# Performance work log

Hardware: AMD Instinct MI355X
Metric: run time of the kernel (lower is better)

## Reference

```python
import jax, jax.numpy as jnp
import numpy as np

N, H, D = 1024, 64, 3

def _lin(x, W, b=None):
    y = x @ W.T
    return y if b is None else y + b

def setup_inputs() -> dict:
    key = jax.random.key(0)
    ks = jax.random.split(key, 16)
    def gl(k, o, i):  # glorot-ish linear weight
        lim = (6.0 / (i + o)) ** 0.5
        return jax.random.uniform(k, (o, i), minval=-lim, maxval=lim, dtype=jnp.float32)
    inp = {
        "h": jax.random.normal(ks[0], (N, H), dtype=jnp.float32),
        "x": jax.random.uniform(ks[1], (N, D), dtype=jnp.float32),  # coords in [0, L)
        "L": jnp.float32(1.0),
        # edge MLP: (2H+2) -> H -> H, silu both layers
        "ew1": gl(ks[2], H, 2 * H + 2), "eb1": jnp.zeros((H,), jnp.float32),
        "ew2": gl(ks[3], H, H),         "eb2": jnp.zeros((H,), jnp.float32),
        # node MLP: 2H -> H -> H
        "nw1": gl(ks[4], H, 2 * H),     "nb1": jnp.zeros((H,), jnp.float32),
        "nw2": gl(ks[5], H, H),         "nb2": jnp.zeros((H,), jnp.float32),
        # coord path
        "chw": gl(ks[6], H, H),         "chb": jnp.zeros((H,), jnp.float32),
        "cww": 0.001 * gl(ks[7], 1, H),  # small-init, no bias
        # attention gate
        "aw": gl(ks[8], 1, H),          "ab": jnp.zeros((1,), jnp.float32),
    }
    return inp

COORDS_RANGE = 10.0

def reference(h, x, L, ew1, eb1, ew2, eb2, nw1, nb1, nw2, nb2, chw, chb, cww, aw, ab):
    act = jax.nn.silu
    n, hd = h.shape
    # --- coord2radial: toroidal log map, x_i - x_j wrapped to [-L/2, L/2) ---
    diff = jnp.remainder(x[:, None, :] - x[None, :, :] + 0.5 * L, L) - 0.5 * L  # (N,N,D)
    radial = jnp.sum(diff ** 2, axis=-1, keepdims=True)                          # (N,N,1)
    coord_diff = diff / (jnp.sqrt(radial + 1e-8) + 1.0)                          # (N,N,D)
    # --- edge model: MLP([h_i, h_j, r, r]) decomposed to avoid concat ---
    Wa, Wb = ew1[:, :hd], ew1[:, hd:2 * hd]
    wr = ew1[:, 2 * hd] + ew1[:, 2 * hd + 1]                                     # (H,)
    pre = (h @ Wa.T)[:, None, :] + (h @ Wb.T)[None, :, :] + radial * wr + eb1    # (N,N,H)
    edge = act(act(pre) @ ew2.T + eb2)                                           # (N,N,H)
    att = jax.nn.sigmoid(edge @ aw.T + ab)                                       # (N,N,1)
    edge = edge * att
    # --- coord model ---
    ch = act(edge @ chw.T + chb)                                                 # (N,N,H)
    w = jnp.tanh(ch @ cww.T) * COORDS_RANGE                                      # (N,N,1)
    delta = jnp.sum(coord_diff * w, axis=1)                                      # (N,D)
    x_new = jnp.remainder(x + delta, L)
    # --- node model ---
    agg = jnp.sum(edge, axis=1)                                                  # (N,H)
    pre_n = h @ nw1[:, :hd].T + agg @ nw1[:, hd:].T + nb1
    h_new = h + (act(pre_n) @ nw2.T + nb2)                                       # recurrent
    return (h_new, x_new)
```

## Files before the change

### kernel.cpp

```cpp
#include <hip/hip_runtime.h>

#define Nn 1024

typedef __attribute__((ext_vector_type(8))) short short8v;
typedef __attribute__((ext_vector_type(4))) float floatx4;

__device__ __forceinline__ float frcp(float v)  { return __builtin_amdgcn_rcpf(v); }
__device__ __forceinline__ float fsilu(float v) { return v * frcp(1.0f + __expf(-v)); }
__device__ __forceinline__ float fsig(float v)  { return frcp(1.0f + __expf(-v)); }
__device__ __forceinline__ float ftanh10(float v){ return 10.0f - 20.0f * frcp(__expf(2.0f * v) + 1.0f); }

__device__ __forceinline__ unsigned cvtpk(float lo, float hi) {
    unsigned r;
    asm("v_cvt_pk_bf16_f32 %0, %1, %2" : "=v"(r) : "v"(lo), "v"(hi));
    return r;
}

union I4S8 { int4 i; short8v s; };

__global__ __launch_bounds__(256) void precompute_kernel(
    const float* __restrict__ h, const float* __restrict__ ew1,
    const float* __restrict__ eb1, const float* __restrict__ nw1,
    const float* __restrict__ nb1, float* __restrict__ ha,
    float* __restrict__ hb, float* __restrict__ hn1)
{
    int t = blockIdx.x * 256 + threadIdx.x;
    int which = t >> 16;
    int rem = t & 65535;
    int i = rem >> 6, o = rem & 63;
    const float* hrow = h + i * 64;
    const float* wrow;
    float acc;
    if (which == 0)      { wrow = ew1 + o * 130;      acc = eb1[o]; }
    else if (which == 1) { wrow = ew1 + o * 130 + 64; acc = 0.0f;   }
    else                 { wrow = nw1 + o * 128;      acc = nb1[o]; }
    #pragma unroll
    for (int k = 0; k < 64; ++k) acc = fmaf(hrow[k], wrow[k], acc);
    if (which == 0)      ha[rem]  = acc;
    else if (which == 1) hb[rem]  = acc;
    else                 hn1[rem] = acc;
}

__global__ __launch_bounds__(256) __attribute__((amdgpu_waves_per_eu(3, 4)))
void edge_mfma_kernel(
    const float* __restrict__ x, const float* __restrict__ Lp,
    const float* __restrict__ ha, const float* __restrict__ hb,
    const float* __restrict__ ew1, const float* __restrict__ ew2,
    const float* __restrict__ eb2, const float* __restrict__ chw,
    const float* __restrict__ chb, const float* __restrict__ aw,
    const float* __restrict__ ab, const float* __restrict__ cww,
    float* __restrict__ agg, float* __restrict__ delta)
{
    __shared__ __align__(16) int4 Wlds[1024];
    __shared__ __align__(16) float cvec[384];
    __shared__ __align__(16) float xs[Nn * 3];
    __shared__ float redagg[4][64];
    __shared__ float sdel[4][3];

    const int tid  = threadIdx.x;
    const int wave = tid >> 6, lane = tid & 63;
    const int lr = lane & 15, g = lane >> 4;
    const int i0 = blockIdx.x;
    const int jbase = wave * 256;
    const int ghi  = g >> 1;
    const int selA = (lr + ((g & 1) << 5)) << 2;
    const int selB = selA + 64;
    const int4* WldsF = &Wlds[0];

    {
        const float4* xsrc = (const float4*)x;
        float4* xdst = (float4*)xs;
        xdst[tid] = xsrc[tid];
        xdst[tid + 256] = xsrc[tid + 256];
        xdst[tid + 512] = xsrc[tid + 512];
    }

    if (wave == 0) {
      #pragma unroll
      for (int kt = 0; kt < 2; ++kt)
        #pragma unroll
        for (int nt = 0; nt < 4; ++nt) {
          int n = nt * 16 + lr;
          int k0 = kt * 32 + g * 8;
          float4 lo = *(const float4*)(ew2 + n * 64 + k0);
          float4 hi = *(const float4*)(ew2 + n * 64 + k0 + 4);
          Wlds[(kt * 4 + nt) * 64 + lane] = make_int4(
              (int)cvtpk(lo.x, lo.y), (int)cvtpk(lo.z, lo.w),
              (int)cvtpk(hi.x, hi.y), (int)cvtpk(hi.z, hi.w));
          lo = *(const float4*)(chw + n * 64 + k0);
          hi = *(const float4*)(chw + n * 64 + k0 + 4);
          Wlds[512 + (kt * 4 + nt) * 64 + lane] = make_int4(
              (int)cvtpk(lo.x, lo.y), (int)cvtpk(lo.z, lo.w),
              (int)cvtpk(hi.x, hi.y), (int)cvtpk(hi.z, hi.w));
        }
    }
    if (tid < 64) {
      cvec[tid]       = eb2[tid];
      cvec[64 + tid]  = aw[tid];
      cvec[128 + tid] = chb[tid];
      cvec[192 + tid] = cww[tid];
      cvec[256 + tid] = ha[i0 * 64 + tid];
      cvec[320 + tid] = ew1[tid * 130 + 128] + ew1[tid * 130 + 129];
    }

    const float L = Lp[0], invL = frcp(L);
    const float ab0 = ab[0];

    floatx4 agg4[4];
    #pragma unroll
    for (int nt = 0; nt < 4; ++nt) agg4[nt] = (floatx4){0.f, 0.f, 0.f, 0.f};
    float dp0 = 0.f, dp1 = 0.f, dp2 = 0.f;

    __syncthreads();

    const float xi0 = xs[i0 * 3 + 0], xi1 = xs[i0 * 3 + 1], xi2 = xs[i0 * 3 + 2];

    float4 hpre0, hpre1, hpre2, hpre3;
    {
      const float* hn = hb + (jbase + lr) * 64 + g * 8;
      hpre0 = *(const float4*)(hn);
      hpre1 = *(const float4*)(hn + 4);
      hpre2 = *(const float4*)(hn + 32);
      hpre3 = *(const float4*)(hn + 36);
    }

    for (int jc = 0; jc < 16; ++jc) {
      unsigned lidx = (unsigned)lane;
      asm volatile("" : "+v"(lidx));
      unsigned cb = (unsigned)(g << 4);
      asm volatile("" : "+v"(cb));
      unsigned hbo = (unsigned)(g << 5);
      asm volatile("" : "+v"(hbo));
      const float* cvp = (const float*)((const char*)cvec + cb);
      const float* hvp = (const float*)((const char*)cvec + 1024 + hbo);

      float4 h0 = hpre0, h1 = hpre1, h2 = hpre2, h3 = hpre3;
      if (jc < 15) {
        const float* hn = hb + (jbase + (jc + 1) * 16 + lr) * 64 + g * 8;
        hpre0 = *(const float4*)(hn);
        hpre1 = *(const float4*)(hn + 4);
        hpre2 = *(const float4*)(hn + 32);
        hpre3 = *(const float4*)(hn + 36);
      }

      const int j = jbase + jc * 16 + lr;
      float xd0 = xi0 - xs[j * 3 + 0];
      float xd1 = xi1 - xs[j * 3 + 1];
      float xd2 = xi2 - xs[j * 3 + 2];
      float d0 = xd0 - L * floorf(fmaf(xd0, invL, 0.5f));
      float d1 = xd1 - L * floorf(fmaf(xd1, invL, 0.5f));
      float d2 = xd2 - L * floorf(fmaf(xd2, invL, 0.5f));
      float radial = d0 * d0 + d1 * d1 + d2 * d2;
      float cinv = frcp(__builtin_amdgcn_sqrtf(radial + 1e-8f) + 1.0f);
      float dx0 = d0 * cinv, dx1 = d1 * cinv, dx2 = d2 * cinv;

      short8v tf[2];
      {
        union { short8v s; unsigned u[4]; } pk;
        #pragma unroll
        for (int kt = 0; kt < 2; ++kt) {
          floatx4 ha0 = *(const floatx4*)(hvp + kt * 32);
          floatx4 ha1 = *(const floatx4*)(hvp + kt * 32 + 4);
          floatx4 wr0 = *(const floatx4*)(hvp + 64 + kt * 32);
          floatx4 wr1 = *(const floatx4*)(hvp + 64 + kt * 32 + 4);
          const float4& hA = kt ? h2 : h0;
          const float4& hB = kt ? h3 : h1;
          floatx4 p0, p1;
          p0[0] = fsilu(fmaf(radial, wr0[0], ha0[0]) + hA.x);
          p0[1] = fsilu(fmaf(radial, wr0[1], ha0[1]) + hA.y);
          p0[2] = fsilu(fmaf(radial, wr0[2], ha0[2]) + hA.z);
          p0[3] = fsilu(fmaf(radial, wr0[3], ha0[3]) + hA.w);
          p1[0] = fsilu(fmaf(radial, wr1[0], ha1[0]) + hB.x);
          p1[1] = fsilu(fmaf(radial, wr1[1], ha1[1]) + hB.y);
          p1[2] = fsilu(fmaf(radial, wr1[2], ha1[2]) + hB.z);
          p1[3] = fsilu(fmaf(radial, wr1[3], ha1[3]) + hB.w);
          pk.u[0] = cvtpk(p0[0], p0[1]); pk.u[1] = cvtpk(p0[2], p0[3]);
          pk.u[2] = cvtpk(p1[0], p1[1]); pk.u[3] = cvtpk(p1[2], p1[3]);
          tf[kt] = pk.s;
        }
      }

      floatx4 acc[4];
      #pragma unroll
      for (int nt = 0; nt < 4; ++nt) acc[nt] = *(const floatx4*)(cvp + nt * 16);
      #pragma unroll
      for (int kt = 0; kt < 2; ++kt)
        #pragma unroll
        for (int nt = 0; nt < 4; ++nt) {
          I4S8 wv; wv.i = WldsF[(kt * 4 + nt) * 64 + lidx];
          acc[nt] = __builtin_amdgcn_mfma_f32_16x16x32_bf16(wv.s, tf[kt], acc[nt], 0, 0, 0);
        }

      float p = 0.f;
      #pragma unroll
      for (int nt = 0; nt < 4; ++nt) {
        floatx4 awv = *(const floatx4*)(cvp + 64 + nt * 16);
        #pragma unroll
        for (int r = 0; r < 4; ++r) {
          float s = fsilu(acc[nt][r]);
          acc[nt][r] = s;
          p = fmaf(s, awv[r], p);
        }
      }
      p += __shfl_xor(p, 16); p += __shfl_xor(p, 32);
      const float att = fsig(p + ab0);

      unsigned Pq[4][2];
      #pragma unroll
      for (int nt = 0; nt < 4; ++nt) {
        float e0 = acc[nt][0] * att, e1 = acc[nt][1] * att;
        float e2 = acc[nt][2] * att, e3 = acc[nt][3] * att;
        agg4[nt][0] += e0; agg4[nt][1] += e1;
        agg4[nt][2] += e2; agg4[nt][3] += e3;
        Pq[nt][0] = cvtpk(e0, e1);
        Pq[nt][1] = cvtpk(e2, e3);
      }

      union { short8v s; int u[4]; } ef[2];
      #pragma unroll
      for (int kt2 = 0; kt2 < 2; ++kt2)
        #pragma unroll
        for (int w = 0; w < 4; ++w) {
          int sel = (w < 2) ? selA : selB;
          int v0 = __builtin_amdgcn_ds_bpermute(sel, (int)Pq[kt2 * 2][w & 1]);
          int v1 = __builtin_amdgcn_ds_bpermute(sel, (int)Pq[kt2 * 2 + 1][w & 1]);
          ef[kt2].u[w] = ghi ? v1 : v0;
        }

      #pragma unroll
      for (int nt = 0; nt < 4; ++nt) acc[nt] = *(const floatx4*)(cvp + 128 + nt * 16);
      #pragma unroll
      for (int kt2 = 0; kt2 < 2; ++kt2)
        #pragma unroll
        for (int nt = 0; nt < 4; ++nt) {
          I4S8 wv; wv.i = WldsF[512 + (kt2 * 4 + nt) * 64 + lidx];
          acc[nt] = __builtin_amdgcn_mfma_f32_16x16x32_bf16(wv.s, ef[kt2].s, acc[nt], 0, 0, 0);
        }

      float q = 0.f;
      #pragma unroll
      for (int nt = 0; nt < 4; ++nt) {
        floatx4 cwv = *(const floatx4*)(cvp + 192 + nt * 16);
        #pragma unroll
        for (int r = 0; r < 4; ++r)
          q = fmaf(fsilu(acc[nt][r]), cwv[r], q);
      }
      q += __shfl_xor(q, 16); q += __shfl_xor(q, 32);
      const float wvv = ftanh10(q);
      if (g == 0) {
        dp0 = fmaf(dx0, wvv, dp0);
        dp1 = fmaf(dx1, wvv, dp1);
        dp2 = fmaf(dx2, wvv, dp2);
      }
    }

    #pragma unroll
    for (int nt = 0; nt < 4; ++nt)
      #pragma unroll
      for (int r = 0; r < 4; ++r) {
        float v = agg4[nt][r];
        v += __shfl_xor(v, 1); v += __shfl_xor(v, 2);
        v += __shfl_xor(v, 4); v += __shfl_xor(v, 8);
        agg4[nt][r] = v;
      }
    if (lr == 0) {
      #pragma unroll
      for (int nt = 0; nt < 4; ++nt)
        *(floatx4*)&redagg[wave][nt * 16 + (g << 2)] = agg4[nt];
    }
    dp0 += __shfl_xor(dp0, 1); dp0 += __shfl_xor(dp0, 2); dp0 += __shfl_xor(dp0, 4); dp0 += __shfl_xor(dp0, 8);
    dp1 += __shfl_xor(dp1, 1); dp1 += __shfl_xor(dp1, 2); dp1 += __shfl_xor(dp1, 4); dp1 += __shfl_xor(dp1, 8);
    dp2 += __shfl_xor(dp2, 1); dp2 += __shfl_xor(dp2, 2); dp2 += __shfl_xor(dp2, 4); dp2 += __shfl_xor(dp2, 8);
    if (lane == 0) { sdel[wave][0] = dp0; sdel[wave][1] = dp1; sdel[wave][2] = dp2; }
    __syncthreads();
    if (tid < 64)
      agg[i0 * 64 + tid] = redagg[0][tid] + redagg[1][tid] + redagg[2][tid] + redagg[3][tid];
    else if (tid < 67) {
      int d = tid - 64;
      delta[i0 * 3 + d] = sdel[0][d] + sdel[1][d] + sdel[2][d] + sdel[3][d];
    }
}

__global__ __launch_bounds__(256) void node_fused_kernel(
    const float* __restrict__ h, const float* __restrict__ hn1,
    const float* __restrict__ agg, const float* __restrict__ nw1,
    const float* __restrict__ nw2, const float* __restrict__ nb2,
    const float* __restrict__ x, const float* __restrict__ delta,
    const float* __restrict__ Lp, float* __restrict__ outh,
    float* __restrict__ outx)
{
    __shared__ float sps[256];
    const int b = blockIdx.x, tid = threadIdx.x;
    const int gt = b * 256 + tid;
    const int i = gt >> 6, o = gt & 63;
    const float* arow = agg + i * 64;
    const float* wrow = nw1 + o * 128 + 64;
    float acc = hn1[gt];
    #pragma unroll
    for (int k = 0; k < 64; ++k) acc = fmaf(arow[k], wrow[k], acc);
    sps[tid] = fsilu(acc);
    __syncthreads();
    const float* srow = sps + (tid & ~63);
    const float* w2row = nw2 + o * 64;
    float acc2 = h[gt] + nb2[o];
    #pragma unroll
    for (int k = 0; k < 64; ++k) acc2 = fmaf(srow[k], w2row[k], acc2);
    outh[gt] = acc2;
    if (tid < 12) {
        int ii = b * 4 + tid / 3, d = tid % 3;
        float L = Lp[0];
        float v = x[ii * 3 + d] + delta[ii * 3 + d];
        outx[ii * 3 + d] = v - L * floorf(v * frcp(L));
    }
}

extern "C" void kernel_launch(void* const* d_in, const int* in_sizes, int n_in,
                              void* d_out, int out_size, void* d_ws, size_t ws_size,
                              hipStream_t stream) {
    const float* h   = (const float*)d_in[0];
    const float* x   = (const float*)d_in[1];
    const float* Lp  = (const float*)d_in[2];
    const float* ew1 = (const float*)d_in[3];
    const float* eb1 = (const float*)d_in[4];
    const float* ew2 = (const float*)d_in[5];
    const float* eb2 = (const float*)d_in[6];
    const float* nw1 = (const float*)d_in[7];
    const float* nb1 = (const float*)d_in[8];
    const float* nw2 = (const float*)d_in[9];
    const float* nb2 = (const float*)d_in[10];
    const float* chw = (const float*)d_in[11];
    const float* chb = (const float*)d_in[12];
    const float* cww = (const float*)d_in[13];
    const float* aw  = (const float*)d_in[14];
    const float* ab  = (const float*)d_in[15];

    float* ws    = (float*)d_ws;
    float* ha    = ws;
    float* hb    = ws + 65536;
    float* hn1   = ws + 131072;
    float* agg   = ws + 196608;
    float* delta = ws + 262144;

    float* outh = (float*)d_out;
    float* outx = outh + 65536;

    precompute_kernel<<<768, 256, 0, stream>>>(h, ew1, eb1, nw1, nb1, ha, hb, hn1);
    edge_mfma_kernel<<<1024, 256, 0, stream>>>(x, Lp, ha, hb, ew1, ew2, eb2, chw, chb,
                                               aw, ab, cww, agg, delta);
    node_fused_kernel<<<256, 256, 0, stream>>>(h, hn1, agg, nw1, nw2, nb2, x, delta,
                                               Lp, outh, outx);
}
```

Measured before the change: 93.31 us.

## Split edge kernel j-range across two blocks per row and drop LDS x staging

```diff
diff --git a/kernel.cpp b/kernel.cpp
--- a/kernel.cpp
+++ b/kernel.cpp
@@ -20,9 +20,8 @@
 
 __global__ __launch_bounds__(256) void precompute_kernel(
     const float* __restrict__ h, const float* __restrict__ ew1,
-    const float* __restrict__ eb1, const float* __restrict__ nw1,
-    const float* __restrict__ nb1, float* __restrict__ ha,
-    float* __restrict__ hb, float* __restrict__ hn1)
+    const float* __restrict__ eb1, float* __restrict__ ha,
+    float* __restrict__ hb)
 {
     int t = blockIdx.x * 256 + threadIdx.x;
     int which = t >> 16;
@@ -31,17 +30,15 @@
     const float* hrow = h + i * 64;
     const float* wrow;
     float acc;
-    if (which == 0)      { wrow = ew1 + o * 130;      acc = eb1[o]; }
-    else if (which == 1) { wrow = ew1 + o * 130 + 64; acc = 0.0f;   }
-    else                 { wrow = nw1 + o * 128;      acc = nb1[o]; }
+    if (which == 0) { wrow = ew1 + o * 130;      acc = eb1[o]; }
+    else            { wrow = ew1 + o * 130 + 64; acc = 0.0f;   }
     #pragma unroll
     for (int k = 0; k < 64; ++k) acc = fmaf(hrow[k], wrow[k], acc);
-    if (which == 0)      ha[rem]  = acc;
-    else if (which == 1) hb[rem]  = acc;
-    else                 hn1[rem] = acc;
-}
-
-__global__ __launch_bounds__(256) __attribute__((amdgpu_waves_per_eu(3, 4)))
+    if (which == 0) ha[rem] = acc;
+    else            hb[rem] = acc;
+}
+
+__global__ __launch_bounds__(256) __attribute__((amdgpu_waves_per_eu(4, 8)))
 void edge_mfma_kernel(
     const float* __restrict__ x, const float* __restrict__ Lp,
     const float* __restrict__ ha, const float* __restrict__ hb,
@@ -49,31 +46,23 @@
     const float* __restrict__ eb2, const float* __restrict__ chw,
     const float* __restrict__ chb, const float* __restrict__ aw,
     const float* __restrict__ ab, const float* __restrict__ cww,
-    float* __restrict__ agg, float* __restrict__ delta)
+    float* __restrict__ agg_parts, float* __restrict__ delta_parts)
 {
     __shared__ __align__(16) int4 Wlds[1024];
     __shared__ __align__(16) float cvec[384];
-    __shared__ __align__(16) float xs[Nn * 3];
     __shared__ float redagg[4][64];
     __shared__ float sdel[4][3];
 
     const int tid  = threadIdx.x;
     const int wave = tid >> 6, lane = tid & 63;
     const int lr = lane & 15, g = lane >> 4;
-    const int i0 = blockIdx.x;
-    const int jbase = wave * 256;
+    const int i0 = blockIdx.x >> 1;
+    const int half = blockIdx.x & 1;
+    const int jbase = half * 512 + wave * 128;
     const int ghi  = g >> 1;
     const int selA = (lr + ((g & 1) << 5)) << 2;
     const int selB = selA + 64;
     const int4* WldsF = &Wlds[0];
-
-    {
-        const float4* xsrc = (const float4*)x;
-        float4* xdst = (float4*)xs;
-        xdst[tid] = xsrc[tid];
-        xdst[tid + 256] = xsrc[tid + 256];
-        xdst[tid + 512] = xsrc[tid + 512];
-    }
 
     if (wave == 0) {
       #pragma unroll
@@ -113,7 +102,7 @@
 
     __syncthreads();
 
-    const float xi0 = xs[i0 * 3 + 0], xi1 = xs[i0 * 3 + 1], xi2 = xs[i0 * 3 + 2];
+    const float xi0 = x[i0 * 3 + 0], xi1 = x[i0 * 3 + 1], xi2 = x[i0 * 3 + 2];
 
     float4 hpre0, hpre1, hpre2, hpre3;
     {
@@ -124,7 +113,7 @@
       hpre3 = *(const float4*)(hn + 36);
     }
 
-    for (int jc = 0; jc < 16; ++jc) {
+    for (int jc = 0; jc < 8; ++jc) {
       unsigned lidx = (unsigned)lane;
       asm volatile("" : "+v"(lidx));
       unsigned cb = (unsigned)(g << 4);
@@ -135,7 +124,7 @@
       const float* hvp = (const float*)((const char*)cvec + 1024 + hbo);
 
       float4 h0 = hpre0, h1 = hpre1, h2 = hpre2, h3 = hpre3;
-      if (jc < 15) {
+      if (jc < 7) {
         const float* hn = hb + (jbase + (jc + 1) * 16 + lr) * 64 + g * 8;
         hpre0 = *(const float4*)(hn);
         hpre1 = *(const float4*)(hn + 4);
@@ -144,9 +133,9 @@
       }
 
       const int j = jbase + jc * 16 + lr;
-      float xd0 = xi0 - xs[j * 3 + 0];
-      float xd1 = xi1 - xs[j * 3 + 1];
-      float xd2 = xi2 - xs[j * 3 + 2];
+      float xd0 = xi0 - x[j * 3 + 0];
+      float xd1 = xi1 - x[j * 3 + 1];
+      float xd2 = xi2 - x[j * 3 + 2];
       float d0 = xd0 - L * floorf(fmaf(xd0, invL, 0.5f));
       float d1 = xd1 - L * floorf(fmaf(xd1, invL, 0.5f));
       float d2 = xd2 - L * floorf(fmaf(xd2, invL, 0.5f));
@@ -274,18 +263,21 @@
     if (lane == 0) { sdel[wave][0] = dp0; sdel[wave][1] = dp1; sdel[wave][2] = dp2; }
     __syncthreads();
     if (tid < 64)
-      agg[i0 * 64 + tid] = redagg[0][tid] + redagg[1][tid] + redagg[2][tid] + redagg[3][tid];
+      agg_parts[half * 65536 + i0 * 64 + tid] =
+          redagg[0][tid] + redagg[1][tid] + redagg[2][tid] + redagg[3][tid];
     else if (tid < 67) {
       int d = tid - 64;
-      delta[i0 * 3 + d] = sdel[0][d] + sdel[1][d] + sdel[2][d] + sdel[3][d];
+      delta_parts[half * 3072 + i0 * 3 + d] =
+          sdel[0][d] + sdel[1][d] + sdel[2][d] + sdel[3][d];
     }
 }
 
 __global__ __launch_bounds__(256) void node_fused_kernel(
-    const float* __restrict__ h, const float* __restrict__ hn1,
-    const float* __restrict__ agg, const float* __restrict__ nw1,
-    const float* __restrict__ nw2, const float* __restrict__ nb2,
-    const float* __restrict__ x, const float* __restrict__ delta,
+    const float* __restrict__ h, const float* __restrict__ agg0,
+    const float* __restrict__ agg1, const float* __restrict__ nw1,
+    const float* __restrict__ nb1, const float* __restrict__ nw2,
+    const float* __restrict__ nb2, const float* __restrict__ x,
+    const float* __restrict__ delta0, const float* __restrict__ delta1,
     const float* __restrict__ Lp, float* __restrict__ outh,
     float* __restrict__ outx)
 {
@@ -293,11 +285,16 @@
     const int b = blockIdx.x, tid = threadIdx.x;
     const int gt = b * 256 + tid;
     const int i = gt >> 6, o = gt & 63;
-    const float* arow = agg + i * 64;
-    const float* wrow = nw1 + o * 128 + 64;
-    float acc = hn1[gt];
-    #pragma unroll
-    for (int k = 0; k < 64; ++k) acc = fmaf(arow[k], wrow[k], acc);
+    const float* hrow = h + i * 64;
+    const float* w1a = nw1 + o * 128;
+    const float* a0 = agg0 + i * 64;
+    const float* a1 = agg1 + i * 64;
+    const float* w1b = nw1 + o * 128 + 64;
+    float acc = nb1[o];
+    #pragma unroll
+    for (int k = 0; k < 64; ++k) acc = fmaf(hrow[k], w1a[k], acc);
+    #pragma unroll
+    for (int k = 0; k < 64; ++k) acc = fmaf(a0[k] + a1[k], w1b[k], acc);
     sps[tid] = fsilu(acc);
     __syncthreads();
     const float* srow = sps + (tid & ~63);
@@ -309,7 +306,7 @@
     if (tid < 12) {
         int ii = b * 4 + tid / 3, d = tid % 3;
         float L = Lp[0];
-        float v = x[ii * 3 + d] + delta[ii * 3 + d];
+        float v = x[ii * 3 + d] + delta0[ii * 3 + d] + delta1[ii * 3 + d];
         outx[ii * 3 + d] = v - L * floorf(v * frcp(L));
     }
 }
@@ -334,19 +331,20 @@
     const float* aw  = (const float*)d_in[14];
     const float* ab  = (const float*)d_in[15];
 
-    float* ws    = (float*)d_ws;
-    float* ha    = ws;
-    float* hb    = ws + 65536;
-    float* hn1   = ws + 131072;
-    float* agg   = ws + 196608;
-    float* delta = ws + 262144;
+    float* ws     = (float*)d_ws;
+    float* ha     = ws;
+    float* hb     = ws + 65536;
+    float* agg0   = ws + 131072;
+    float* agg1   = ws + 196608;
+    float* delta0 = ws + 262144;
+    float* delta1 = ws + 265216;
 
     float* outh = (float*)d_out;
     float* outx = outh + 65536;
 
-    precompute_kernel<<<768, 256, 0, stream>>>(h, ew1, eb1, nw1, nb1, ha, hb, hn1);
-    edge_mfma_kernel<<<1024, 256, 0, stream>>>(x, Lp, ha, hb, ew1, ew2, eb2, chw, chb,
-                                               aw, ab, cww, agg, delta);
-    node_fused_kernel<<<256, 256, 0, stream>>>(h, hn1, agg, nw1, nw2, nb2, x, delta,
-                                               Lp, outh, outx);
-}
+    precompute_kernel<<<512, 256, 0, stream>>>(h, ew1, eb1, ha, hb);
+    edge_mfma_kernel<<<2048, 256, 0, stream>>>(x, Lp, ha, hb, ew1, ew2, eb2, chw, chb,
+                                               aw, ab, cww, ws + 131072, ws + 262144);
+    node_fused_kernel<<<256, 256, 0, stream>>>(h, agg0, agg1, nw1, nb1, nw2, nb2, x,
+                                               delta0, delta1, Lp, outh, outx);
+}
```

New measurement: 90.78 us. 2.7% less time.
